# Performance work log

Hardware: AMD Instinct MI355X
Metric: run time of the kernel (lower is better)

Reference implementation:

```python
import jax, jax.numpy as jnp
import numpy as np

D_MODEL, D_K, D_V = 1024, 128, 128
B, S = 8, 2048


def setup_inputs() -> dict:
    key = jax.random.key(0)
    k1, k2, k3, k4, k5 = jax.random.split(key, 5)
    x = jax.random.normal(k1, (B, S, D_MODEL), dtype=jnp.float32)
    enc_embed = jax.random.normal(k2, (B, S, D_MODEL), dtype=jnp.float32)
    # xavier_normal-ish init: std = sqrt(2/(fan_in+fan_out))
    W_Q = jax.random.normal(k3, (D_MODEL, D_K), dtype=jnp.float32) * np.sqrt(2.0 / (D_MODEL + D_K))
    W_K = jax.random.normal(k4, (D_MODEL, D_K), dtype=jnp.float32) * np.sqrt(2.0 / (D_MODEL + D_K))
    W_V = jax.random.normal(k5, (D_MODEL, D_V), dtype=jnp.float32) * np.sqrt(2.0 / (D_MODEL + D_V))
    return {"x": x, "enc_embed": enc_embed, "W_Q": W_Q, "W_K": W_K, "W_V": W_V}


def reference(x, enc_embed, W_Q, W_K, W_V):
    # use_enc_embed=False, use_mask=False path (self-attention)
    q = jnp.einsum('bsd,dk->bsk', x, W_Q)  # [B,S,d_k]
    k = jnp.einsum('bsd,dk->bsk', x, W_K)  # [B,S,d_k]
    v = jnp.einsum('bsd,dv->bsv', x, W_V)  # [B,S,d_v]
    scale = 1.0 / jnp.sqrt(jnp.asarray(D_K, dtype=x.dtype))
    scores = jnp.einsum('bqk,bsk->bqs', q, k) * scale  # [B,S,S]
    weights = jax.nn.softmax(scores, axis=-1)
    return jnp.einsum('bqs,bsv->bqv', weights, v)  # [B,S,d_v]
```

## Files before the change

### kernel.cpp

```cpp
#include <hip/hip_runtime.h>
#include <hip/hip_bf16.h>
#include <stdint.h>

typedef __attribute__((ext_vector_type(8))) short bf16x8;
typedef __attribute__((ext_vector_type(4))) float f32x4;
typedef __attribute__((ext_vector_type(4))) unsigned short u16x4;
typedef unsigned short u16;

#define D_MODEL 1024
#define DK 128
#define BATCH 8
#define SEQ 2048
#define NROWS (BATCH * SEQ)
#define NSPLIT 4
#define KVPB 512
#define NIT 16

static __device__ __forceinline__ void gl_lds16(const void* g, void* l) {
  __builtin_amdgcn_global_load_lds((const __attribute__((address_space(1))) void*)g,
                                   (__attribute__((address_space(3))) void*)l, 16, 0, 0);
}

static __device__ __forceinline__ u16 f2b(float f) {
  __hip_bfloat16 h = __float2bfloat16(f);
  return *reinterpret_cast<u16*>(&h);
}

static __device__ __forceinline__ uint32_t cvtpk(float lo, float hi) {
  uint32_t r;
  asm("v_cvt_pk_bf16_f32 %0, %1, %2" : "=v"(r) : "v"(lo), "v"(hi));
  return r;
}

static __device__ __forceinline__ float exp2hw(float x) {
  float r;
  asm("v_exp_f32 %0, %1" : "=v"(r) : "v"(x));
  return r;
}

__global__ __launch_bounds__(256) void wcvt(const float* __restrict__ wq,
                                            const float* __restrict__ wk,
                                            const float* __restrict__ wv,
                                            u16* __restrict__ wt2) {
  const int idx = blockIdx.x * 256 + threadIdx.x;
  int w = idx >> 17, rr = idx & 131071, k = rr >> 7, n = rr & 127;
  const float* W = (w == 0) ? wq : ((w == 1) ? wk : wv);
  int np = w * 128 + n;
  int kt = k >> 5;
  int slot = ((k >> 3) & 3) ^ ((np >> 1) & 3);
  size_t dst = ((size_t)kt * 1536 + np * 4 + slot) * 8 + (k & 7);
  wt2[dst] = f2b(W[k * DK + n]);
}

__global__ __launch_bounds__(512, 1) void qkv_gemm(const float* __restrict__ x,
                                                   const u16* __restrict__ wt2,
                                                   u16* __restrict__ qb,
                                                   u16* __restrict__ kb,
                                                   u16* __restrict__ vt) {
  __shared__ char sm[98304] __attribute__((aligned(16)));
  const int tid = threadIdx.x;
  const int lane = tid & 63;
  const int w = tid >> 6;
  const int g = lane >> 4;
  const int l15 = lane & 15;
  const int mt = blockIdx.x;
  const int wm = w >> 2, wn = w & 3;

  const char* aB = (const char*)x + (size_t)mt * 64 * 4096;
  const char* bB = (const char*)wt2;

  f32x4 acc[2][6];
#pragma unroll
  for (int i = 0; i < 2; ++i)
#pragma unroll
    for (int jj = 0; jj < 6; ++jj) acc[i][jj] = (f32x4){0.f, 0.f, 0.f, 0.f};

  auto stage = [&](int buf, int kt) {
    char* sA = sm + buf * 32768;
    char* sB = sA + 8192;
    {
      int row = tid >> 3;
      int gq = (tid & 7) ^ (row & 7);
      gl_lds16(aB + (size_t)row * 4096 + kt * 128 + (gq << 4), sA + w * 1024);
    }
    const char* bSrc = bB + (size_t)kt * 24576;
#pragma unroll
    for (int c = 0; c < 3; ++c) {
      gl_lds16(bSrc + (c * 512 + tid) * 16, sB + c * 8192 + w * 1024);
    }
  };

  auto compute = [&](const char* base) {
    const char* sA = base;
    const char* sB = base + 8192;
    bf16x8 af[2];
#pragma unroll
    for (int mi = 0; mi < 2; ++mi) {
      int row = wm * 32 + mi * 16 + l15;
      f32x4 lo = *(const f32x4*)(sA + row * 128 + ((((2 * g + 0) ^ (row & 7))) << 4));
      f32x4 hi = *(const f32x4*)(sA + row * 128 + ((((2 * g + 1) ^ (row & 7))) << 4));
      union { uint32_t u[4]; bf16x8 v; } tt;
      tt.u[0] = cvtpk(lo[0], lo[1]);
      tt.u[1] = cvtpk(lo[2], lo[3]);
      tt.u[2] = cvtpk(hi[0], hi[1]);
      tt.u[3] = cvtpk(hi[2], hi[3]);
      af[mi] = tt.v;
    }
    bf16x8 bfr[6];
#pragma unroll
    for (int ni = 0; ni < 6; ++ni) {
      int np = wn * 96 + ni * 16 + l15;
      bfr[ni] = *(const bf16x8*)(sB + np * 64 + ((g ^ ((np >> 1) & 3)) << 4));
    }
    __builtin_amdgcn_s_setprio(1);
#pragma unroll
    for (int mi = 0; mi < 2; ++mi)
#pragma unroll
      for (int ni = 0; ni < 6; ++ni)
        acc[mi][ni] = __builtin_amdgcn_mfma_f32_16x16x32_bf16(af[mi], bfr[ni], acc[mi][ni], 0, 0, 0);
    __builtin_amdgcn_s_setprio(0);
  };

  stage(0, 0);
  stage(1, 1);
  int cb = 0;
#pragma unroll 1
  for (int t = 0; t < 32; ++t) {
    if (t < 31) asm volatile("s_waitcnt vmcnt(4)" ::: "memory");
    else asm volatile("s_waitcnt vmcnt(0)" ::: "memory");
    __builtin_amdgcn_s_barrier();
    if (t + 2 < 32) {
      int sb = cb + 2;
      if (sb >= 3) sb -= 3;
      stage(sb, t + 2);
    }
    compute(sm + cb * 32768);
    cb = (cb == 2) ? 0 : cb + 1;
  }

  const float qscale = 0.12751743f;
#pragma unroll
  for (int mi = 0; mi < 2; ++mi) {
#pragma unroll
    for (int ni = 0; ni < 6; ++ni) {
      int mbase = mt * 64 + wm * 32 + mi * 16 + g * 4;
      int np = wn * 96 + ni * 16 + l15;
      int ntd = np >> 7, n = np & 127;
      if (ntd == 2) {
        int b = mbase >> 11, s = mbase & 2047;
        int a = (s >> 2) & 7;
        int sp2 = (s & ~31) | ((((a & 3) << 1) | (a >> 2)) << 2);
        union { u16 u[4]; u16x4 v; } pk;
#pragma unroll
        for (int r2 = 0; r2 < 4; ++r2) pk.u[r2] = f2b(acc[mi][ni][r2]);
        *(u16x4*)((char*)vt + ((size_t)(b * 128 + n) * 2048 + sp2) * 2) = pk.v;
      } else {
        u16* dst = (ntd == 0) ? qb : kb;
        float sc = (ntd == 0) ? qscale : 1.0f;
#pragma unroll
        for (int r2 = 0; r2 < 4; ++r2)
          dst[(size_t)(mbase + r2) * 128 + n] = f2b(acc[mi][ni][r2] * sc);
      }
    }
  }
}

__global__ __launch_bounds__(256) void attn(const u16* __restrict__ qb,
                                            const u16* __restrict__ kb,
                                            const u16* __restrict__ vtg,
                                            u16* __restrict__ po,
                                            float* __restrict__ ls) {
  __shared__ char sm[49152] __attribute__((aligned(16)));
  const int tid = threadIdx.x, lane = tid & 63, w = tid >> 6;
  const int g = lane >> 4, l15 = lane & 15;
  const int id = blockIdx.x;
  const int wgid = ((id & 7) << 6) | (id >> 3);
  const int b = wgid >> 6, sp = (wgid >> 4) & 3, j = wgid & 15;
  const int s0q = j * 128 + w * 32;
  const int kv0 = sp * KVPB;

  const char* qB = (const char*)qb + (size_t)b * SEQ * 256;
  const char* kB = (const char*)kb + (size_t)b * SEQ * 256;
  const char* vB = (const char*)vtg + (size_t)b * 128 * SEQ * 2;

  bf16x8 qf[2][4];
#pragma unroll
  for (int h = 0; h < 2; ++h)
#pragma unroll
    for (int kk = 0; kk < 4; ++kk)
      qf[h][kk] = *(const bf16x8*)(qB + (size_t)(s0q + h * 16 + l15) * 256 + kk * 64 + g * 16);

  f32x4 o[2][8];
#pragma unroll
  for (int h = 0; h < 2; ++h)
#pragma unroll
    for (int i = 0; i < 8; ++i) o[h][i] = (f32x4){0.f, 0.f, 0.f, 0.f};
  float lsum[2] = {0.f, 0.f};

  char* sKb = sm;
  char* sVb = sm + 24576;

  auto stage = [&](int bi, int it) {
    char* sK = sKb + bi * 8192;
    char* sV = sVb + bi * 8192;
    int s0 = kv0 + it * 32;
#pragma unroll
    for (int c = 0; c < 2; ++c) {
      int base = c * 4096 + w * 1024;
      int L = base + lane * 16;
      {
        int row = L >> 8, col = L & 255;
        gl_lds16(kB + (size_t)(s0 + row) * 256 + (col ^ ((row & 7) << 4)), sK + base);
      }
      {
        int rv = L >> 6, cv = L & 63;
        gl_lds16(vB + (size_t)rv * 4096 + (size_t)s0 * 2 + (cv ^ ((rv & 3) << 4)), sV + base);
      }
    }
  };

  stage(0, 0);
  stage(1, 1);
  int cb = 0;
  for (int t = 0; t < NIT; ++t) {
    if (t < NIT - 1) asm volatile("s_waitcnt vmcnt(4)" ::: "memory");
    else asm volatile("s_waitcnt vmcnt(0)" ::: "memory");
    __builtin_amdgcn_s_barrier();
    if (t + 2 < NIT) {
      int sb = cb + 2;
      if (sb >= 3) sb -= 3;
      stage(sb, t + 2);
    }
    const char* sK = sKb + cb * 8192;
    const char* sV = sVb + cb * 8192;

    f32x4 st[2][2];
    st[0][0] = (f32x4){0.f, 0.f, 0.f, 0.f}; st[0][1] = st[0][0];
    st[1][0] = st[0][0]; st[1][1] = st[0][0];
    __builtin_amdgcn_s_setprio(1);
#pragma unroll
    for (int sub = 0; sub < 2; ++sub)
#pragma unroll
      for (int kk = 0; kk < 4; ++kk) {
        bf16x8 kf = *(const bf16x8*)(sK + (sub * 16 + l15) * 256 +
                                     ((kk * 64 + g * 16) ^ ((l15 & 7) << 4)));
        st[0][sub] = __builtin_amdgcn_mfma_f32_16x16x32_bf16(kf, qf[0][kk], st[0][sub], 0, 0, 0);
        st[1][sub] = __builtin_amdgcn_mfma_f32_16x16x32_bf16(kf, qf[1][kk], st[1][sub], 0, 0, 0);
      }
    __builtin_amdgcn_s_setprio(0);

    union U { uint32_t u[4]; bf16x8 v; } pf[2];
#pragma unroll
    for (int h = 0; h < 2; ++h) {
      float p[8];
#pragma unroll
      for (int sub = 0; sub < 2; ++sub)
#pragma unroll
        for (int r2 = 0; r2 < 4; ++r2) {
          float e = exp2hw(st[h][sub][r2]);
          lsum[h] += e;
          p[sub * 4 + r2] = e;
        }
      pf[h].u[0] = cvtpk(p[0], p[1]);
      pf[h].u[1] = cvtpk(p[2], p[3]);
      pf[h].u[2] = cvtpk(p[4], p[5]);
      pf[h].u[3] = cvtpk(p[6], p[7]);
    }

    __builtin_amdgcn_s_setprio(1);
#pragma unroll
    for (int dsub = 0; dsub < 8; ++dsub) {
      bf16x8 vf = *(const bf16x8*)(sV + (dsub * 16 + l15) * 64 +
                                   ((g * 16) ^ ((l15 & 3) << 4)));
      o[0][dsub] = __builtin_amdgcn_mfma_f32_16x16x32_bf16(vf, pf[0].v, o[0][dsub], 0, 0, 0);
      o[1][dsub] = __builtin_amdgcn_mfma_f32_16x16x32_bf16(vf, pf[1].v, o[1][dsub], 0, 0, 0);
    }
    __builtin_amdgcn_s_setprio(0);
    cb = (cb == 2) ? 0 : cb + 1;
  }

#pragma unroll
  for (int h = 0; h < 2; ++h) {
    lsum[h] += __shfl_xor(lsum[h], 16);
    lsum[h] += __shfl_xor(lsum[h], 32);
    int ridx = (b * 16 + j) * 128 + w * 32 + h * 16 + l15;
    u16* dst = po + ((size_t)sp * NROWS + ridx) * 128;
#pragma unroll
    for (int dsub = 0; dsub < 8; ++dsub) {
      union { uint32_t u[2]; u16x4 v; } pk2;
      pk2.u[0] = cvtpk(o[h][dsub][0], o[h][dsub][1]);
      pk2.u[1] = cvtpk(o[h][dsub][2], o[h][dsub][3]);
      *(u16x4*)(dst + dsub * 16 + g * 4) = pk2.v;
    }
    if (g == 0) ls[(size_t)sp * NROWS + ridx] = lsum[h];
  }
}

__global__ __launch_bounds__(256) void attn_combine(const u16* __restrict__ po,
                                                    const float* __restrict__ ls,
                                                    float* __restrict__ out) {
  int idx = blockIdx.x * 256 + threadIdx.x;
  int r = idx >> 4, d0 = (idx & 15) * 8;
  float denom = 0.f;
  float acc[8];
#pragma unroll
  for (int j = 0; j < 8; ++j) acc[j] = 0.f;
#pragma unroll
  for (int s = 0; s < NSPLIT; ++s) {
    denom += ls[(size_t)s * NROWS + r];
    bf16x8 v = *(const bf16x8*)(po + ((size_t)s * NROWS + r) * 128 + d0);
#pragma unroll
    for (int j = 0; j < 8; ++j) {
      uint32_t bits = ((uint32_t)(u16)v[j]) << 16;
      acc[j] += *reinterpret_cast<float*>(&bits);
    }
  }
  float inv = 1.0f / denom;
  f32x4 o0 = (f32x4){acc[0], acc[1], acc[2], acc[3]};
  f32x4 o1 = (f32x4){acc[4], acc[5], acc[6], acc[7]};
  *(f32x4*)(out + (size_t)r * 128 + d0) = o0 * inv;
  *(f32x4*)(out + (size_t)r * 128 + d0 + 4) = o1 * inv;
}

extern "C" void kernel_launch(void* const* d_in, const int* in_sizes, int n_in,
                              void* d_out, int out_size, void* d_ws, size_t ws_size,
                              hipStream_t stream) {
  const float* x = (const float*)d_in[0];
  const float* wq = (const float*)d_in[2];
  const float* wk = (const float*)d_in[3];
  const float* wv = (const float*)d_in[4];

  char* ws = (char*)d_ws;
  u16* po = (u16*)ws;
  float* ls = (float*)(ws + 16777216);
  u16* wt2 = (u16*)(ws + 17039360);
  u16* qb = (u16*)(ws + 17825792);
  u16* kb = (u16*)(ws + 22020096);
  u16* vt = (u16*)(ws + 26214400);
  float* out = (float*)d_out;

  wcvt<<<dim3(1536), dim3(256), 0, stream>>>(wq, wk, wv, wt2);
  qkv_gemm<<<dim3(256), dim3(512), 0, stream>>>(x, wt2, qb, kb, vt);
  attn<<<dim3(512), dim3(256), 0, stream>>>(qb, kb, vt, po, ls);
  attn_combine<<<dim3(1024), dim3(256), 0, stream>>>(po, ls, out);
}
```

Baseline: 63.01 us.

## Double K-tile depth in QKV GEMM with two-stage double buffering

```diff
diff --git a/kernel.cpp b/kernel.cpp
--- a/kernel.cpp
+++ b/kernel.cpp
@@ -41,23 +41,23 @@
 __global__ __launch_bounds__(256) void wcvt(const float* __restrict__ wq,
                                             const float* __restrict__ wk,
                                             const float* __restrict__ wv,
-                                            u16* __restrict__ wt2) {
+                                            u16* __restrict__ wt3) {
   const int idx = blockIdx.x * 256 + threadIdx.x;
   int w = idx >> 17, rr = idx & 131071, k = rr >> 7, n = rr & 127;
   const float* W = (w == 0) ? wq : ((w == 1) ? wk : wv);
   int np = w * 128 + n;
-  int kt = k >> 5;
-  int slot = ((k >> 3) & 3) ^ ((np >> 1) & 3);
-  size_t dst = ((size_t)kt * 1536 + np * 4 + slot) * 8 + (k & 7);
-  wt2[dst] = f2b(W[k * DK + n]);
+  int kt = k >> 6;
+  int slot = ((k >> 3) & 7) ^ ((np >> 1) & 7);
+  size_t dst = ((size_t)kt * 3072 + np * 8 + slot) * 8 + (k & 7);
+  wt3[dst] = f2b(W[k * DK + n]);
 }
 
 __global__ __launch_bounds__(512, 1) void qkv_gemm(const float* __restrict__ x,
-                                                   const u16* __restrict__ wt2,
+                                                   const u16* __restrict__ wt3,
                                                    u16* __restrict__ qb,
                                                    u16* __restrict__ kb,
                                                    u16* __restrict__ vt) {
-  __shared__ char sm[98304] __attribute__((aligned(16)));
+  __shared__ char sm[131072] __attribute__((aligned(16)));
   const int tid = threadIdx.x;
   const int lane = tid & 63;
   const int w = tid >> 6;
@@ -67,7 +67,7 @@
   const int wm = w >> 2, wn = w & 3;
 
   const char* aB = (const char*)x + (size_t)mt * 64 * 4096;
-  const char* bB = (const char*)wt2;
+  const char* bB = (const char*)wt3;
 
   f32x4 acc[2][6];
 #pragma unroll
@@ -76,66 +76,74 @@
     for (int jj = 0; jj < 6; ++jj) acc[i][jj] = (f32x4){0.f, 0.f, 0.f, 0.f};
 
   auto stage = [&](int buf, int kt) {
-    char* sA = sm + buf * 32768;
-    char* sB = sA + 8192;
-    {
-      int row = tid >> 3;
-      int gq = (tid & 7) ^ (row & 7);
-      gl_lds16(aB + (size_t)row * 4096 + kt * 128 + (gq << 4), sA + w * 1024);
-    }
-    const char* bSrc = bB + (size_t)kt * 24576;
-#pragma unroll
-    for (int c = 0; c < 3; ++c) {
+    char* sA = sm + buf * 65536;
+    char* sB = sA + 16384;
+#pragma unroll
+    for (int c = 0; c < 2; ++c) {
+      int si = c * 512 + tid;
+      int row = si >> 4;
+      int s = si & 15;
+      int gq = (s & 8) | ((s & 7) ^ (row & 7));
+      gl_lds16(aB + (size_t)row * 4096 + kt * 256 + (gq << 4), sA + c * 8192 + w * 1024);
+    }
+    const char* bSrc = bB + (size_t)kt * 49152;
+#pragma unroll
+    for (int c = 0; c < 6; ++c) {
       gl_lds16(bSrc + (c * 512 + tid) * 16, sB + c * 8192 + w * 1024);
     }
   };
 
   auto compute = [&](const char* base) {
     const char* sA = base;
-    const char* sB = base + 8192;
-    bf16x8 af[2];
-#pragma unroll
-    for (int mi = 0; mi < 2; ++mi) {
-      int row = wm * 32 + mi * 16 + l15;
-      f32x4 lo = *(const f32x4*)(sA + row * 128 + ((((2 * g + 0) ^ (row & 7))) << 4));
-      f32x4 hi = *(const f32x4*)(sA + row * 128 + ((((2 * g + 1) ^ (row & 7))) << 4));
-      union { uint32_t u[4]; bf16x8 v; } tt;
-      tt.u[0] = cvtpk(lo[0], lo[1]);
-      tt.u[1] = cvtpk(lo[2], lo[3]);
-      tt.u[2] = cvtpk(hi[0], hi[1]);
-      tt.u[3] = cvtpk(hi[2], hi[3]);
-      af[mi] = tt.v;
-    }
-    bf16x8 bfr[6];
-#pragma unroll
-    for (int ni = 0; ni < 6; ++ni) {
-      int np = wn * 96 + ni * 16 + l15;
-      bfr[ni] = *(const bf16x8*)(sB + np * 64 + ((g ^ ((np >> 1) & 3)) << 4));
-    }
-    __builtin_amdgcn_s_setprio(1);
-#pragma unroll
-    for (int mi = 0; mi < 2; ++mi)
-#pragma unroll
-      for (int ni = 0; ni < 6; ++ni)
-        acc[mi][ni] = __builtin_amdgcn_mfma_f32_16x16x32_bf16(af[mi], bfr[ni], acc[mi][ni], 0, 0, 0);
-    __builtin_amdgcn_s_setprio(0);
+    const char* sB = base + 16384;
+#pragma unroll
+    for (int kk = 0; kk < 2; ++kk) {
+      bf16x8 af[2];
+#pragma unroll
+      for (int mi = 0; mi < 2; ++mi) {
+        int row = wm * 32 + mi * 16 + l15;
+        f32x4 lo = *(const f32x4*)(sA + row * 256 +
+                                   (((kk * 8) | ((2 * g + 0) ^ (row & 7))) << 4));
+        f32x4 hi = *(const f32x4*)(sA + row * 256 +
+                                   (((kk * 8) | ((2 * g + 1) ^ (row & 7))) << 4));
+        union { uint32_t u[4]; bf16x8 v; } tt;
+        tt.u[0] = cvtpk(lo[0], lo[1]);
+        tt.u[1] = cvtpk(lo[2], lo[3]);
+        tt.u[2] = cvtpk(hi[0], hi[1]);
+        tt.u[3] = cvtpk(hi[2], hi[3]);
+        af[mi] = tt.v;
+      }
+      bf16x8 bfr[6];
+#pragma unroll
+      for (int ni = 0; ni < 6; ++ni) {
+        int np = wn * 96 + ni * 16 + l15;
+        bfr[ni] = *(const bf16x8*)(sB + np * 128 +
+                                   (((kk * 4 + g) ^ ((np >> 1) & 7)) << 4));
+      }
+      __builtin_amdgcn_s_setprio(1);
+#pragma unroll
+      for (int mi = 0; mi < 2; ++mi)
+#pragma unroll
+        for (int ni = 0; ni < 6; ++ni)
+          acc[mi][ni] = __builtin_amdgcn_mfma_f32_16x16x32_bf16(af[mi], bfr[ni], acc[mi][ni], 0, 0, 0);
+      __builtin_amdgcn_s_setprio(0);
+    }
   };
 
   stage(0, 0);
-  stage(1, 1);
-  int cb = 0;
 #pragma unroll 1
-  for (int t = 0; t < 32; ++t) {
-    if (t < 31) asm volatile("s_waitcnt vmcnt(4)" ::: "memory");
-    else asm volatile("s_waitcnt vmcnt(0)" ::: "memory");
+  for (int t = 0; t < 16; ++t) {
+    if (t < 15) {
+      stage((t + 1) & 1, t + 1);
+      asm volatile("s_waitcnt vmcnt(8)" ::: "memory");
+    } else {
+      asm volatile("s_waitcnt vmcnt(0)" ::: "memory");
+    }
     __builtin_amdgcn_s_barrier();
-    if (t + 2 < 32) {
-      int sb = cb + 2;
-      if (sb >= 3) sb -= 3;
-      stage(sb, t + 2);
-    }
-    compute(sm + cb * 32768);
-    cb = (cb == 2) ? 0 : cb + 1;
+    asm volatile("" ::: "memory");
+    compute(sm + (t & 1) * 65536);
+    asm volatile("" ::: "memory");
+    __builtin_amdgcn_s_barrier();
   }
 
   const float qscale = 0.12751743f;
@@ -333,14 +341,14 @@
   char* ws = (char*)d_ws;
   u16* po = (u16*)ws;
   float* ls = (float*)(ws + 16777216);
-  u16* wt2 = (u16*)(ws + 17039360);
+  u16* wt3 = (u16*)(ws + 17039360);
   u16* qb = (u16*)(ws + 17825792);
   u16* kb = (u16*)(ws + 22020096);
   u16* vt = (u16*)(ws + 26214400);
   float* out = (float*)d_out;
 
-  wcvt<<<dim3(1536), dim3(256), 0, stream>>>(wq, wk, wv, wt2);
-  qkv_gemm<<<dim3(256), dim3(512), 0, stream>>>(x, wt2, qb, kb, vt);
+  wcvt<<<dim3(1536), dim3(256), 0, stream>>>(wq, wk, wv, wt3);
+  qkv_gemm<<<dim3(256), dim3(512), 0, stream>>>(x, wt3, qb, kb, vt);
   attn<<<dim3(512), dim3(256), 0, stream>>>(qb, kb, vt, po, ls);
   attn_combine<<<dim3(1024), dim3(256), 0, stream>>>(po, ls, out);
 }
```

Result: no change. 63.78 us (+1.2%).
